# Optimization experiments

Measured on AMD Instinct MI355X. Metric: run time of the kernel, lower is better.

The kernel has to match this reference:

```python
import jax, jax.numpy as jnp
import numpy as np

DIM = 512
HEADS = 8
HD = DIM // HEADS
B, T, N = 4, 64, 196
HIDDEN = 2048  # dim * ffn_ratio
SCALE = HD ** -0.5
EPS = 1e-5


def _ln(x, g, b):
    m = jnp.mean(x, axis=-1, keepdims=True)
    v = jnp.mean(jnp.square(x - m), axis=-1, keepdims=True)
    return (x - m) / jnp.sqrt(v + EPS) * g + b


def _attn(x, qkv_w, q_b, v_b, proj_w, proj_b, mask=None):
    # x: [B', T', N', C]; attention over the N' axis
    Bp, Tp, Np, C = x.shape
    bias = jnp.concatenate([q_b, jnp.zeros_like(v_b), v_b])  # torch cat(q_bias, zeros, v_bias)
    qkv = x @ qkv_w.T + bias                                  # [B',T',N',3C]
    qkv = qkv.reshape(Bp, Tp, Np, 3, HEADS, HD).transpose(3, 0, 1, 4, 2, 5)
    q, k, v = qkv[0] * SCALE, qkv[1], qkv[2]                  # [B',T',H,N',hd]
    attn = jnp.einsum('bthnd,bthmd->bthnm', q, k)             # [B',T',H,N',N']
    if mask is not None:
        attn = attn + mask                                    # broadcast [N',N'] bias
    attn = jax.nn.softmax(attn, axis=-1)
    out = jnp.einsum('bthnm,bthmd->bthnd', attn, v)
    out = out.transpose(0, 1, 3, 2, 4).reshape(Bp, Tp, Np, C)
    return out @ proj_w.T + proj_b


def setup_inputs() -> dict:
    key = jax.random.key(0)
    ks = jax.random.split(key, 16)
    w = lambda k, s: (0.02 * jax.random.normal(k, s)).astype(jnp.float32)
    return {
        'x': jax.random.normal(ks[0], (B, T, N, DIM), dtype=jnp.float32),
        'mask': 0.1 * jax.random.normal(ks[1], (T, T), dtype=jnp.float32),
        'n1_g': jnp.ones((DIM,), jnp.float32),
        'n1_b': jnp.zeros((DIM,), jnp.float32),
        's_qkv_w': w(ks[2], (3 * DIM, DIM)),
        's_q_b': jnp.zeros((DIM,), jnp.float32),
        's_v_b': jnp.zeros((DIM,), jnp.float32),
        's_proj_w': w(ks[3], (DIM, DIM)),
        's_proj_b': jnp.zeros((DIM,), jnp.float32),
        't_qkv_w': w(ks[4], (3 * DIM, DIM)),
        't_q_b': jnp.zeros((DIM,), jnp.float32),
        't_v_b': jnp.zeros((DIM,), jnp.float32),
        't_proj_w': w(ks[5], (DIM, DIM)),
        't_proj_b': jnp.zeros((DIM,), jnp.float32),
        'n2_g': jnp.ones((DIM,), jnp.float32),
        'n2_b': jnp.zeros((DIM,), jnp.float32),
        'ffn_w1': w(ks[6], (HIDDEN, DIM)),
        'ffn_b1': jnp.zeros((HIDDEN,), jnp.float32),
        'ffn_w2': w(ks[7], (DIM, HIDDEN)),
        'ffn_b2': jnp.zeros((DIM,), jnp.float32),
    }


def reference(x, mask, n1_g, n1_b, s_qkv_w, s_q_b, s_v_b, s_proj_w, s_proj_b,
              t_qkv_w, t_q_b, t_v_b, t_proj_w, t_proj_b,
              n2_g, n2_b, ffn_w1, ffn_b1, ffn_w2, ffn_b2):
    h = _ln(x, n1_g, n1_b)
    sp = _attn(h, s_qkv_w, s_q_b, s_v_b, s_proj_w, s_proj_b)
    # temporal branch: transpose (B,T,N,C) -> (B,N,T,C); mask [T,T] biases the T x T scores
    tm = _attn(h.transpose(0, 2, 1, 3), t_qkv_w, t_q_b, t_v_b, t_proj_w, t_proj_b, mask)
    tm = tm.transpose(0, 2, 1, 3)
    x = x + 0.5 * sp + 0.5 * tm
    h2 = _ln(x, n2_g, n2_b)
    ffn = jax.nn.gelu(h2 @ ffn_w1.T + ffn_b1, approximate=False) @ ffn_w2.T + ffn_b2
    return x + ffn
```

## Files before the change

kernel.cpp:

```cpp
#include <hip/hip_runtime.h>
#include <cmath>

typedef unsigned short u16;
typedef __bf16 bf16x8 __attribute__((ext_vector_type(8)));
typedef float f32x4 __attribute__((ext_vector_type(4)));

__device__ __forceinline__ float bflo(unsigned u){ return __uint_as_float(u << 16); }
__device__ __forceinline__ float bfhi(unsigned u){ return __uint_as_float(u & 0xffff0000u); }
__device__ __forceinline__ float b2f(u16 b){ return __uint_as_float(((unsigned)b) << 16); }
__device__ __forceinline__ u16 f2bf(float f){
  unsigned u = __float_as_uint(f);
  u = u + 0x7fffu + ((u >> 16) & 1u);
  return (u16)(u >> 16);
}
__device__ __forceinline__ unsigned pk2(float a, float b){
  return (unsigned)f2bf(a) | ((unsigned)f2bf(b) << 16);
}
__device__ __forceinline__ void up8(uint4 u, float* f){
  f[0]=bflo(u.x); f[1]=bfhi(u.x); f[2]=bflo(u.y); f[3]=bfhi(u.y);
  f[4]=bflo(u.z); f[5]=bfhi(u.z); f[6]=bflo(u.w); f[7]=bfhi(u.w);
}
__device__ __forceinline__ float rdd(const void* p, int f, size_t i){
  return f ? ((const float*)p)[i] : b2f(((const u16*)p)[i]);
}
__device__ __forceinline__ float erf_fast(float x){
  const float ax = fabsf(x);
  const float t  = __builtin_amdgcn_rcpf(1.f + 0.3275911f * ax);
  float p = 1.061405429f;
  p = p * t - 1.453152027f;
  p = p * t + 1.421413741f;
  p = p * t - 0.284496736f;
  p = p * t + 0.254829592f;
  const float e = __expf(-ax * ax);
  const float r = 1.f - p * t * e;
  return copysignf(r, x);
}
__device__ __forceinline__ void gload16(const u16* g, u16* l){
  __builtin_amdgcn_global_load_lds(
      (const __attribute__((address_space(1))) void*)g,
      (__attribute__((address_space(3))) void*)l, 16, 0, 0);
}

__global__ void detect_k(const unsigned* __restrict__ n1g, int* __restrict__ flag){
  if (threadIdx.x == 0 && blockIdx.x == 0)
    *flag = (n1g[0] == 0x3F800000u) ? 1 : 0;
}

__global__ void conv_k(const void* __restrict__ src, u16* __restrict__ dst, int n,
                       const int* __restrict__ flag){
  const int f = *flag;
  const int i = blockIdx.x * 256 + threadIdx.x;
  if (i >= n) return;
  dst[i] = f ? f2bf(((const float*)src)[i]) : ((const u16*)src)[i];
}

__global__ void conv_multi(const void* a0, const void* a1, const void* a2, const void* a3,
                           const void* a4, const void* a5, const void* a6, const void* a7,
                           const void* a8, const void* a9, const void* aa, const void* ab,
                           const void* ac, u16* __restrict__ dst, const int* __restrict__ flag){
  const int f = *flag;
  const int i = blockIdx.x * 256 + threadIdx.x;
  if (i >= 11776) return;
  const void* s; int o;
  if      (i < 2048)  { s = a0; o = i; }
  else if (i < 2560)  { s = a1; o = i - 2048; }
  else if (i < 3072)  { s = a2; o = i - 2560; }
  else if (i < 3584)  { s = a3; o = i - 3072; }
  else if (i < 4096)  { s = a4; o = i - 3584; }
  else if (i < 4608)  { s = a5; o = i - 4096; }
  else if (i < 8704)  { s = a6; o = i - 4608; }
  else if (i < 9216)  { s = a7; o = i - 8704; }
  else if (i < 9728)  { s = a8; o = i - 9216; }
  else if (i < 10240) { s = a9; o = i - 9728; }
  else if (i < 10752) { s = aa; o = i - 10240; }
  else if (i < 11264) { s = ab; o = i - 10752; }
  else                { s = ac; o = i - 11264; }
  dst[i] = f ? f2bf(((const float*)s)[o]) : ((const u16*)s)[o];
}

__global__ void build_bias(const u16* __restrict__ sqb, const u16* __restrict__ svb,
                           const u16* __restrict__ tqb, const u16* __restrict__ tvb,
                           u16* __restrict__ dst){
  int i = blockIdx.x * 256 + threadIdx.x;
  if (i >= 1536) return;
  u16 s, t;
  if (i < 512)       { s = sqb[i];       t = tqb[i]; }
  else if (i < 1024) { s = 0;            t = 0; }
  else               { s = svb[i-1024];  t = tvb[i-1024]; }
  dst[i] = s; dst[1536 + i] = t;
}

__global__ void build_cproj(const void* __restrict__ sp, const void* __restrict__ tp,
                            const void* __restrict__ spb, const void* __restrict__ tpb,
                            u16* __restrict__ wc, u16* __restrict__ cb,
                            const int* __restrict__ flag){
  const int f = *flag;
  const int i = blockIdx.x * 256 + threadIdx.x;
  if (i < 524288){
    const int n = i >> 10, k = i & 1023;
    const float v = (k < 512) ? rdd(sp, f, (size_t)n*512 + k)
                              : rdd(tp, f, (size_t)n*512 + k - 512);
    wc[i] = f2bf(v);
  }
  if (i < 512) cb[i] = f2bf(rdd(spb, f, i) + rdd(tpb, f, i));
}

__global__ __launch_bounds__(256) void ln_k(const void* __restrict__ x, int rowbase,
                                            const u16* __restrict__ g, const u16* __restrict__ b,
                                            u16* __restrict__ out, const int* __restrict__ flagp){
  const int f = *flagp;
  const int gw   = (blockIdx.x * 256 + threadIdx.x) >> 6;
  const int lane = threadIdx.x & 63;
  const size_t base = (size_t)(rowbase + gw) * 512 + lane * 8;
  float fv[8];
  if (f){
    const float4* p = (const float4*)((const float*)x + base);
    float4 a = p[0], c = p[1];
    fv[0]=a.x; fv[1]=a.y; fv[2]=a.z; fv[3]=a.w;
    fv[4]=c.x; fv[5]=c.y; fv[6]=c.z; fv[7]=c.w;
  } else {
    up8(*(const uint4*)((const u16*)x + base), fv);
  }
  float s1 = 0.f, s2 = 0.f;
  #pragma unroll
  for (int i = 0; i < 8; i++){ s1 += fv[i]; s2 += fv[i]*fv[i]; }
  #pragma unroll
  for (int off = 32; off > 0; off >>= 1){
    s1 += __shfl_xor(s1, off, 64);
    s2 += __shfl_xor(s2, off, 64);
  }
  const float mean = s1 * (1.f/512.f);
  const float var  = fmaxf(s2 * (1.f/512.f) - mean*mean, 0.f);
  const float inv  = rsqrtf(var + 1e-5f);
  float gg[8], bb[8];
  up8(*(const uint4*)&g[lane*8], gg);
  up8(*(const uint4*)&b[lane*8], bb);
  float r[8];
  #pragma unroll
  for (int i = 0; i < 8; i++) r[i] = (fv[i]-mean)*inv*gg[i] + bb[i];
  uint4 o;
  o.x = pk2(r[0],r[1]); o.y = pk2(r[2],r[3]); o.z = pk2(r[4],r[5]); o.w = pk2(r[6],r[7]);
  *(uint4*)&out[(size_t)gw*512 + lane*8] = o;
}

template<int EPI, int IO>
__global__ __launch_bounds__(512, 6) void gemm_bt(
    const u16* __restrict__ A, const u16* __restrict__ W, int ldw,
    const u16* __restrict__ bias, const void* __restrict__ res,
    void* __restrict__ out, int rowbase, int N, int K, const int* __restrict__ flagp)
{
  __shared__ u16 sA[2][128 * 32];
  __shared__ u16 sB[2][128 * 32];
  const int f = (IO == 1) ? *flagp : 0;
  const int tid  = threadIdx.x;
  const int wave = tid >> 6, lane = tid & 63;
  const int wm   = (wave >> 1) * 32;
  const int wn   = (wave & 1) * 64;
  const int col0 = blockIdx.x * 128, row0 = blockIdx.y * 128;

  f32x4 acc[2][4];
  const f32x4 z = {0.f, 0.f, 0.f, 0.f};
  #pragma unroll
  for (int i = 0; i < 2; i++)
    #pragma unroll
    for (int j = 0; j < 4; j++) acc[i][j] = z;

  const int srow = (wave << 4) + (lane >> 2);
  const int scol = (lane & 3) * 8;
  const u16* Ag = A + (size_t)(row0 + srow) * K   + scol;
  const u16* Wg = W + (size_t)(col0 + srow) * ldw + scol;
  const int wofs = wave << 9;
  const int ks = (lane >> 4) * 8, mr = lane & 15;

  #define STAGE(bb, kk) do {                    \
    gload16(Ag + (kk), &sA[bb][wofs]);          \
    gload16(Wg + (kk), &sB[bb][wofs]);          \
  } while (0)

  const int nit = K >> 5;
  STAGE(0, 0);
  for (int it = 0; it < nit; ++it){
    const int b = it & 1;
    if (it + 1 < nit){
      STAGE(b ^ 1, (it + 1) << 5);
      asm volatile("s_waitcnt vmcnt(2)" ::: "memory");
    } else {
      asm volatile("s_waitcnt vmcnt(0)" ::: "memory");
    }
    __builtin_amdgcn_s_barrier();
    bf16x8 af[2], bq[4];
    #pragma unroll
    for (int i = 0; i < 2; i++)
      af[i] = *(const bf16x8*)&sA[b][(wm + i*16 + mr)*32 + ks];
    #pragma unroll
    for (int j = 0; j < 4; j++)
      bq[j] = *(const bf16x8*)&sB[b][(wn + j*16 + mr)*32 + ks];
    #pragma unroll
    for (int i = 0; i < 2; i++)
      #pragma unroll
      for (int j = 0; j < 4; j++)
        acc[i][j] = __builtin_amdgcn_mfma_f32_16x16x32_bf16(bq[j], af[i], acc[i][j], 0, 0, 0);
    __builtin_amdgcn_s_barrier();
  }
  #undef STAGE

  #pragma unroll
  for (int i = 0; i < 2; i++){
    const int m = row0 + wm + i*16 + mr;
    const size_t rowoff = (size_t)(rowbase + m) * N;
    #pragma unroll
    for (int j = 0; j < 4; j++){
      const int n0 = col0 + wn + j*16 + (lane >> 4)*4;
      const uint2 bb = *(const uint2*)&bias[n0];
      float v[4];
      v[0] = acc[i][j][0] + bflo(bb.x);
      v[1] = acc[i][j][1] + bfhi(bb.x);
      v[2] = acc[i][j][2] + bflo(bb.y);
      v[3] = acc[i][j][3] + bfhi(bb.y);
      if (EPI == 1 || EPI == 3){
        float r4[4];
        if (f){
          const float4 rr = *(const float4*)((const float*)res + rowoff + n0);
          r4[0]=rr.x; r4[1]=rr.y; r4[2]=rr.z; r4[3]=rr.w;
        } else {
          const uint2 ru = *(const uint2*)((const u16*)res + rowoff + n0);
          r4[0]=bflo(ru.x); r4[1]=bfhi(ru.x); r4[2]=bflo(ru.y); r4[3]=bfhi(ru.y);
        }
        #pragma unroll
        for (int t = 0; t < 4; t++)
          v[t] = (EPI == 1) ? r4[t] + 0.5f * v[t] : r4[t] + v[t];
      } else if (EPI == 2){
        #pragma unroll
        for (int t = 0; t < 4; t++)
          v[t] = 0.5f * v[t] * (1.f + erf_fast(v[t] * 0.70710678f));
      }
      if (IO == 0 || !f){
        uint2 o; o.x = pk2(v[0], v[1]); o.y = pk2(v[2], v[3]);
        *(uint2*)((u16*)out + rowoff + n0) = o;
      } else {
        float4 o = {v[0], v[1], v[2], v[3]};
        *(float4*)((float*)out + rowoff + n0) = o;
      }
    }
  }
}

#define VSTR 232
__global__ __launch_bounds__(256) void attn_spatial_mfma(const u16* __restrict__ qkv, int rstr,
                                                         u16* __restrict__ ao, int ostr){
  __shared__ u16 Vt[64 * VSTR];
  __shared__ u16 Ps[4][16 * VSTR];
  const int btl = blockIdx.x, h = blockIdx.y;
  const u16* base = qkv + (size_t)btl * 196 * rstr + h * 64;
  const int tid = threadIdx.x, wave = tid >> 6, lane = tid & 63;
  const f32x4 z4 = {0.f, 0.f, 0.f, 0.f};

  for (int tsk = tid; tsk < 1568; tsk += 256){
    const int m = tsk >> 3, d8 = (tsk & 7) * 8;
    float vf[8];
    up8(*(const uint4*)&base[(size_t)m*rstr + 1024 + d8], vf);
    #pragma unroll
    for (int j = 0; j < 8; j++) Vt[(d8 + j)*VSTR + m] = f2bf(vf[j]);
  }
  for (int tsk = tid; tsk < 64*28; tsk += 256){
    const int d = tsk / 28, m = 196 + (tsk - d*28);
    Vt[d*VSTR + m] = 0;
  }
  __syncthreads();

  const int li = lane & 15, q8 = (lane >> 4) * 8;
  for (int p = 0; p < 4; p++){
    const int rt = p*4 + wave;
    if (rt > 12) continue;
    const int row0 = rt * 16;
    const int qrc = min(row0 + li, 195);
    const u16* qp = base + (size_t)qrc*rstr + q8;
    const bf16x8 q0 = *(const bf16x8*)qp;
    const bf16x8 q1 = *(const bf16x8*)(qp + 32);

    f32x4 acc[14];
    #pragma unroll
    for (int mt = 0; mt < 14; mt++) acc[mt] = z4;
    #pragma unroll
    for (int mt = 0; mt < 14; mt++){
      const int krc = min(mt*16 + li, 195);
      const u16* kp = base + (size_t)krc*rstr + 512 + q8;
      const bf16x8 k0 = *(const bf16x8*)kp;
      const bf16x8 k1 = *(const bf16x8*)(kp + 32);
      acc[mt] = __builtin_amdgcn_mfma_f32_16x16x32_bf16(q0, k0, acc[mt], 0, 0, 0);
      acc[mt] = __builtin_amdgcn_mfma_f32_16x16x32_bf16(q1, k1, acc[mt], 0, 0, 0);
    }
    float den[4];
    #pragma unroll
    for (int rr = 0; rr < 4; rr++){
      float mx = -1.0e30f;
      #pragma unroll
      for (int mt = 0; mt < 14; mt++){
        float s = acc[mt][rr] * 0.125f;
        if (mt*16 + li >= 196) s = -1.0e30f;
        acc[mt][rr] = s;
        mx = fmaxf(mx, s);
      }
      #pragma unroll
      for (int off = 1; off < 16; off <<= 1) mx = fmaxf(mx, __shfl_xor(mx, off, 64));
      float d = 0.f;
      #pragma unroll
      for (int mt = 0; mt < 14; mt++){
        const float pv = __expf(acc[mt][rr] - mx);
        acc[mt][rr] = pv;
        d += pv;
      }
      #pragma unroll
      for (int off = 1; off < 16; off <<= 1) d += __shfl_xor(d, off, 64);
      den[rr] = d;
    }
    u16* ps = &Ps[wave][0];
    #pragma unroll
    for (int rr = 0; rr < 4; rr++){
      const int prow = (lane >> 4)*4 + rr;
      #pragma unroll
      for (int mt = 0; mt < 14; mt++)
        ps[prow*VSTR + mt*16 + li] = f2bf(acc[mt][rr]);
    }
    f32x4 ov[4];
    #pragma unroll
    for (int nt = 0; nt < 4; nt++) ov[nt] = z4;
    #pragma unroll
    for (int kk = 0; kk < 7; kk++){
      const bf16x8 pf = *(const bf16x8*)&ps[li*VSTR + kk*32 + q8];
      #pragma unroll
      for (int nt = 0; nt < 4; nt++){
        const bf16x8 vb = *(const bf16x8*)&Vt[(nt*16 + li)*VSTR + kk*32 + q8];
        ov[nt] = __builtin_amdgcn_mfma_f32_16x16x32_bf16(pf, vb, ov[nt], 0, 0, 0);
      }
    }
    #pragma unroll
    for (int rr = 0; rr < 4; rr++){
      const int row = row0 + (lane >> 4)*4 + rr;
      if (row < 196){
        const float inv = 1.f / den[rr];
        u16* orow = ao + ((size_t)btl*196 + row)*ostr + h*64;
        #pragma unroll
        for (int nt = 0; nt < 4; nt++)
          orow[nt*16 + li] = f2bf(ov[nt][rr] * inv);
      }
    }
  }
}

#define TSTR 72
__global__ __launch_bounds__(256) void attn_temporal_mfma(const u16* __restrict__ qkv, int rstr,
                                                          const u16* __restrict__ mask,
                                                          u16* __restrict__ ao, int ostr){
  __shared__ u16 Ks[64 * TSTR];
  __shared__ u16 Vt[64 * TSTR];
  __shared__ u16 Mk[64 * TSTR];
  __shared__ u16 Ps[4][16 * TSTR];
  const int n = blockIdx.x, h = blockIdx.y, bz = blockIdx.z;
  const int tid = threadIdx.x, wave = tid >> 6, lane = tid & 63;
  const size_t trow = (size_t)196 * rstr;
  const u16* base = qkv + ((size_t)bz*12544 + n) * rstr + h * 64;
  const f32x4 z4 = {0.f, 0.f, 0.f, 0.f};

  for (int tsk = tid; tsk < 512; tsk += 256){
    const int r = tsk >> 3, c8 = (tsk & 7) * 8;
    *(uint4*)&Ks[r*TSTR + c8] = *(const uint4*)&base[(size_t)r*trow + 512 + c8];
    *(uint4*)&Mk[r*TSTR + c8] = *(const uint4*)&mask[r*64 + c8];
    float vf[8];
    up8(*(const uint4*)&base[(size_t)r*trow + 1024 + c8], vf);
    #pragma unroll
    for (int j = 0; j < 8; j++) Vt[(c8 + j)*TSTR + r] = f2bf(vf[j]);
  }
  __syncthreads();

  const int li = lane & 15, q8 = (lane >> 4) * 8;
  const int row0 = wave * 16;
  const u16* qp = base + (size_t)(row0 + li)*trow + q8;
  const bf16x8 q0 = *(const bf16x8*)qp;
  const bf16x8 q1 = *(const bf16x8*)(qp + 32);

  f32x4 acc[4];
  #pragma unroll
  for (int mt = 0; mt < 4; mt++) acc[mt] = z4;
  #pragma unroll
  for (int mt = 0; mt < 4; mt++){
    const bf16x8 k0 = *(const bf16x8*)&Ks[(mt*16 + li)*TSTR + q8];
    const bf16x8 k1 = *(const bf16x8*)&Ks[(mt*16 + li)*TSTR + 32 + q8];
    acc[mt] = __builtin_amdgcn_mfma_f32_16x16x32_bf16(q0, k0, acc[mt], 0, 0, 0);
    acc[mt] = __builtin_amdgcn_mfma_f32_16x16x32_bf16(q1, k1, acc[mt], 0, 0, 0);
  }
  float den[4];
  #pragma unroll
  for (int rr = 0; rr < 4; rr++){
    const int tq = row0 + (lane >> 4)*4 + rr;
    float mx = -1.0e30f;
    #pragma unroll
    for (int mt = 0; mt < 4; mt++){
      const float s = acc[mt][rr] * 0.125f + b2f(Mk[tq*TSTR + mt*16 + li]);
      acc[mt][rr] = s;
      mx = fmaxf(mx, s);
    }
    #pragma unroll
    for (int off = 1; off < 16; off <<= 1) mx = fmaxf(mx, __shfl_xor(mx, off, 64));
    float d = 0.f;
    #pragma unroll
    for (int mt = 0; mt < 4; mt++){
      const float pv = __expf(acc[mt][rr] - mx);
      acc[mt][rr] = pv;
      d += pv;
    }
    #pragma unroll
    for (int off = 1; off < 16; off <<= 1) d += __shfl_xor(d, off, 64);
    den[rr] = d;
  }
  u16* ps = &Ps[wave][0];
  #pragma unroll
  for (int rr = 0; rr < 4; rr++){
    const int prow = (lane >> 4)*4 + rr;
    #pragma unroll
    for (int mt = 0; mt < 4; mt++)
      ps[prow*TSTR + mt*16 + li] = f2bf(acc[mt][rr]);
  }
  f32x4 ov[4];
  #pragma unroll
  for (int nt = 0; nt < 4; nt++) ov[nt] = z4;
  #pragma unroll
  for (int kk = 0; kk < 2; kk++){
    const bf16x8 pf = *(const bf16x8*)&ps[li*TSTR + kk*32 + q8];
    #pragma unroll
    for (int nt = 0; nt < 4; nt++){
      const bf16x8 vb = *(const bf16x8*)&Vt[(nt*16 + li)*TSTR + kk*32 + q8];
      ov[nt] = __builtin_amdgcn_mfma_f32_16x16x32_bf16(pf, vb, ov[nt], 0, 0, 0);
    }
  }
  #pragma unroll
  for (int rr = 0; rr < 4; rr++){
    const int tq = row0 + (lane >> 4)*4 + rr;
    const float inv = 1.f / den[rr];
    u16* orow = ao + ((size_t)bz*12544 + (size_t)tq*196 + n)*ostr + h*64;
    #pragma unroll
    for (int nt = 0; nt < 4; nt++)
      orow[nt*16 + li] = f2bf(ov[nt][rr] * inv);
  }
}

extern "C" void kernel_launch(void* const* d_in, const int* in_sizes, int n_in,
                              void* d_out, int out_size, void* d_ws, size_t ws_size,
                              hipStream_t stream)
{
  (void)in_sizes; (void)n_in; (void)out_size;
  const void* x = d_in[0];
  void* outp = d_out;

  u16* ws = (u16*)d_ws;
  u16* m_sqkvw = ws;
  u16* m_tqkvw = ws + 786432;
  u16* m_sprojw= ws + 1572864;
  u16* m_tprojw= ws + 1835008;
  u16* m_cprojw= ws + 2097152;
  u16* m_fw1   = ws + 2621440;
  u16* m_fw2   = ws + 3670016;
  u16* m_fb1   = ws + 4718592;
  u16* m_fb2   = ws + 4720640;
  u16* m_n1g   = ws + 4721152;
  u16* m_n1b   = ws + 4721664;
  u16* m_n2g   = ws + 4722176;
  u16* m_n2b   = ws + 4722688;
  u16* m_mask  = ws + 4723200;
  u16* m_sqb   = ws + 4727296;
  u16* m_svb   = ws + 4727808;
  u16* m_tqb   = ws + 4728320;
  u16* m_tvb   = ws + 4728832;
  u16* m_spb   = ws + 4729344;
  u16* m_tpb   = ws + 4729856;
  u16* m_cpb   = ws + 4730368;
  u16* bias2   = ws + 4730880;
  int* flag    = (int*)(ws + 4733952);
  u16* buf     = ws + 4734016;

  const size_t MIR = 4734016;
  #define NEED(CHX) ((MIR + (size_t)(CHX)*4608) * 2)
  int CHX;
  if      (ws_size >= NEED(50176)) CHX = 50176;
  else if (ws_size >= NEED(25088)) CHX = 25088;
  else if (ws_size >= NEED(12544)) CHX = 12544;
  else                             CHX = 0;
  #undef NEED

  detect_k<<<dim3(1), dim3(64), 0, stream>>>((const unsigned*)d_in[2], flag);
  conv_multi<<<dim3(46), dim3(256), 0, stream>>>(
      d_in[17], d_in[19], d_in[2], d_in[3], d_in[14], d_in[15], d_in[1],
      d_in[5], d_in[6], d_in[10], d_in[11], d_in[8], d_in[13], m_fb1, flag);
  #define CONV(idx, dst, n) conv_k<<<dim3(((n)+255)/256), dim3(256), 0, stream>>>(d_in[idx], dst, n, flag)
  CONV(4,  m_sqkvw, 786432);
  CONV(9,  m_tqkvw, 786432);
  CONV(7,  m_sprojw,262144);
  CONV(12, m_tprojw,262144);
  CONV(16, m_fw1,  1048576);
  CONV(18, m_fw2,  1048576);
  #undef CONV
  build_bias<<<dim3(6), dim3(256), 0, stream>>>(m_sqb, m_svb, m_tqb, m_tvb, bias2);
  build_cproj<<<dim3(2048), dim3(256), 0, stream>>>(d_in[7], d_in[12], d_in[8], d_in[13],
                                                    m_cprojw, m_cpb, flag);

  if (CHX > 0){
    const int nb = CHX / 12544;
    const int nc = 50176 / CHX;
    const int gr = CHX / 128;
    const int sp = CHX / 196;
    u16* hc  = buf;
    u16* qq  = buf + (size_t)CHX*512;
    u16* ao  = buf + (size_t)CHX*3584;
    u16* mid = qq;
    for (int c = 0; c < nc; c++){
      const int rb = c * CHX;
      ln_k<<<dim3(CHX/4), dim3(256), 0, stream>>>(x, rb, m_n1g, m_n1b, hc, flag);
      gemm_bt<0,0><<<dim3(24, gr), dim3(512), 0, stream>>>(hc, m_sqkvw, 512, bias2, nullptr, qq, 0, 3072, 512, flag);
      attn_spatial_mfma<<<dim3(sp, 8), dim3(256), 0, stream>>>(qq, 3072, ao, 1024);
      attn_temporal_mfma<<<dim3(196, 8, nb), dim3(256), 0, stream>>>(qq + 1536, 3072, m_mask, ao + 512, 1024);
      gemm_bt<1,1><<<dim3(4, gr), dim3(512), 0, stream>>>(ao, m_cprojw, 1024, m_cpb, x, outp, rb, 512, 1024, flag);
      ln_k<<<dim3(CHX/4), dim3(256), 0, stream>>>(outp, rb, m_n2g, m_n2b, hc, flag);
      gemm_bt<2,0><<<dim3(16, gr), dim3(512), 0, stream>>>(hc, m_fw1, 512, m_fb1, nullptr, mid, 0, 2048, 512, flag);
      gemm_bt<3,1><<<dim3(4, gr), dim3(512), 0, stream>>>(mid, m_fw2, 2048, m_fb2, outp, outp, rb, 512, 2048, flag);
    }
  } else {
    const int CH = 12544;
    u16* hc  = buf;
    u16* Wq  = buf + (size_t)CH*512;
    u16* Wa  = buf + (size_t)CH*2048;
    u16* mid = Wq;
    for (int c = 0; c < 4; c++){
      const int rb = c * CH;
      ln_k<<<dim3(3136), dim3(256), 0, stream>>>(x, rb, m_n1g, m_n1b, hc, flag);
      gemm_bt<0,0><<<dim3(12, 98), dim3(512), 0, stream>>>(hc, m_sqkvw, 512, bias2, nullptr, Wq, 0, 1536, 512, flag);
      attn_spatial_mfma<<<dim3(64, 8), dim3(256), 0, stream>>>(Wq, 1536, Wa, 512);
      gemm_bt<1,1><<<dim3(4, 98), dim3(512), 0, stream>>>(Wa, m_sprojw, 512, m_spb, x, outp, rb, 512, 512, flag);
      gemm_bt<0,0><<<dim3(12, 98), dim3(512), 0, stream>>>(hc, m_tqkvw, 512, bias2 + 1536, nullptr, Wq, 0, 1536, 512, flag);
      attn_temporal_mfma<<<dim3(196, 8, 1), dim3(256), 0, stream>>>(Wq, 1536, m_mask, Wa, 512);
      gemm_bt<1,1><<<dim3(4, 98), dim3(512), 0, stream>>>(Wa, m_tprojw, 512, m_tpb, outp, outp, rb, 512, 512, flag);
      ln_k<<<dim3(3136), dim3(256), 0, stream>>>(outp, rb, m_n2g, m_n2b, hc, flag);
      gemm_bt<2,0><<<dim3(16, 98), dim3(512), 0, stream>>>(hc, m_fw1, 512, m_fb1, nullptr, mid, 0, 2048, 512, flag);
      gemm_bt<3,1><<<dim3(4, 98), dim3(512), 0, stream>>>(mid, m_fw2, 2048, m_fb2, outp, outp, rb, 512, 2048, flag);
    }
  }
}
```

Before: 1.276 ms.

## Enlarge GEMM tile to 256x128 and swizzle LDS columns

The bf16 MFMA GEMM now computes a 256x128 tile per block, so each wave owns a 64x64 sub-tile with 16 accumulators instead of 8, and the grid row count is halved accordingly. This raises arithmetic intensity per LDS fragment load and per global load of the weight tile. An XOR swizzle on the k-column offset within LDS rows is added to reduce bank conflicts on fragment reads. The cost is more registers per thread (launch bounds lowered to 4) and fewer blocks, which can hurt occupancy and tail balance on small grids.

```diff
diff --git a/kernel.cpp b/kernel.cpp
--- a/kernel.cpp
+++ b/kernel.cpp
@@ -144,37 +144,41 @@
 }
 
 template<int EPI, int IO>
-__global__ __launch_bounds__(512, 6) void gemm_bt(
+__global__ __launch_bounds__(512, 4) void gemm_bt(
     const u16* __restrict__ A, const u16* __restrict__ W, int ldw,
     const u16* __restrict__ bias, const void* __restrict__ res,
     void* __restrict__ out, int rowbase, int N, int K, const int* __restrict__ flagp)
 {
-  __shared__ u16 sA[2][128 * 32];
+  __shared__ u16 sA[2][256 * 32];
   __shared__ u16 sB[2][128 * 32];
   const int f = (IO == 1) ? *flagp : 0;
   const int tid  = threadIdx.x;
   const int wave = tid >> 6, lane = tid & 63;
-  const int wm   = (wave >> 1) * 32;
-  const int wn   = (wave & 1) * 64;
-  const int col0 = blockIdx.x * 128, row0 = blockIdx.y * 128;
-
-  f32x4 acc[2][4];
+  const int wr   = (wave >> 1) * 64;
+  const int wc   = (wave & 1) * 64;
+  const int col0 = blockIdx.x * 128, row0 = blockIdx.y * 256;
+
+  f32x4 acc[4][4];
   const f32x4 z = {0.f, 0.f, 0.f, 0.f};
   #pragma unroll
-  for (int i = 0; i < 2; i++)
+  for (int i = 0; i < 4; i++)
     #pragma unroll
     for (int j = 0; j < 4; j++) acc[i][j] = z;
 
-  const int srow = (wave << 4) + (lane >> 2);
-  const int scol = (lane & 3) * 8;
-  const u16* Ag = A + (size_t)(row0 + srow) * K   + scol;
-  const u16* Wg = W + (size_t)(col0 + srow) * ldw + scol;
-  const int wofs = wave << 9;
-  const int ks = (lane >> 4) * 8, mr = lane & 15;
-
-  #define STAGE(bb, kk) do {                    \
-    gload16(Ag + (kk), &sA[bb][wofs]);          \
-    gload16(Wg + (kk), &sB[bb][wofs]);          \
+  const int srow = lane >> 2;
+  const int scol = ((lane & 3) ^ ((lane >> 3) & 3)) * 8;
+  const u16* Ag = A + (size_t)(row0 + (wave << 5) + srow) * K + scol;
+  const u16* Wg = W + (size_t)(col0 + (wave << 4) + srow) * ldw + scol;
+  const size_t ajmp = (size_t)16 * K;
+  const int wofsA = wave << 10;
+  const int wofsB = wave << 9;
+  const int ksw = (((lane >> 4) ^ ((lane >> 1) & 3)) * 8);
+  const int mr = lane & 15;
+
+  #define STAGE(bb, kk) do {                              \
+    gload16(Ag + (kk),        &sA[bb][wofsA]);            \
+    gload16(Ag + (kk) + ajmp, &sA[bb][wofsA + 512]);      \
+    gload16(Wg + (kk),        &sB[bb][wofsB]);            \
   } while (0)
 
   const int nit = K >> 5;
@@ -183,20 +187,20 @@
     const int b = it & 1;
     if (it + 1 < nit){
       STAGE(b ^ 1, (it + 1) << 5);
-      asm volatile("s_waitcnt vmcnt(2)" ::: "memory");
+      asm volatile("s_waitcnt vmcnt(3)" ::: "memory");
     } else {
       asm volatile("s_waitcnt vmcnt(0)" ::: "memory");
     }
     __builtin_amdgcn_s_barrier();
-    bf16x8 af[2], bq[4];
-    #pragma unroll
-    for (int i = 0; i < 2; i++)
-      af[i] = *(const bf16x8*)&sA[b][(wm + i*16 + mr)*32 + ks];
+    bf16x8 af[4], bq[4];
+    #pragma unroll
+    for (int i = 0; i < 4; i++)
+      af[i] = *(const bf16x8*)&sA[b][(wr + i*16 + mr)*32 + ksw];
     #pragma unroll
     for (int j = 0; j < 4; j++)
-      bq[j] = *(const bf16x8*)&sB[b][(wn + j*16 + mr)*32 + ks];
-    #pragma unroll
-    for (int i = 0; i < 2; i++)
+      bq[j] = *(const bf16x8*)&sB[b][(wc + j*16 + mr)*32 + ksw];
+    #pragma unroll
+    for (int i = 0; i < 4; i++)
       #pragma unroll
       for (int j = 0; j < 4; j++)
         acc[i][j] = __builtin_amdgcn_mfma_f32_16x16x32_bf16(bq[j], af[i], acc[i][j], 0, 0, 0);
@@ -205,12 +209,12 @@
   #undef STAGE
 
   #pragma unroll
-  for (int i = 0; i < 2; i++){
-    const int m = row0 + wm + i*16 + mr;
+  for (int i = 0; i < 4; i++){
+    const int m = row0 + wr + i*16 + mr;
     const size_t rowoff = (size_t)(rowbase + m) * N;
     #pragma unroll
     for (int j = 0; j < 4; j++){
-      const int n0 = col0 + wn + j*16 + (lane >> 4)*4;
+      const int n0 = col0 + wc + j*16 + (lane >> 4)*4;
       const uint2 bb = *(const uint2*)&bias[n0];
       float v[4];
       v[0] = acc[i][j][0] + bflo(bb.x);
@@ -506,7 +510,7 @@
   if (CHX > 0){
     const int nb = CHX / 12544;
     const int nc = 50176 / CHX;
-    const int gr = CHX / 128;
+    const int gr = CHX / 256;
     const int sp = CHX / 196;
     u16* hc  = buf;
     u16* qq  = buf + (size_t)CHX*512;
@@ -532,15 +536,15 @@
     for (int c = 0; c < 4; c++){
       const int rb = c * CH;
       ln_k<<<dim3(3136), dim3(256), 0, stream>>>(x, rb, m_n1g, m_n1b, hc, flag);
-      gemm_bt<0,0><<<dim3(12, 98), dim3(512), 0, stream>>>(hc, m_sqkvw, 512, bias2, nullptr, Wq, 0, 1536, 512, flag);
+      gemm_bt<0,0><<<dim3(12, 49), dim3(512), 0, stream>>>(hc, m_sqkvw, 512, bias2, nullptr, Wq, 0, 1536, 512, flag);
       attn_spatial_mfma<<<dim3(64, 8), dim3(256), 0, stream>>>(Wq, 1536, Wa, 512);
-      gemm_bt<1,1><<<dim3(4, 98), dim3(512), 0, stream>>>(Wa, m_sprojw, 512, m_spb, x, outp, rb, 512, 512, flag);
-      gemm_bt<0,0><<<dim3(12, 98), dim3(512), 0, stream>>>(hc, m_tqkvw, 512, bias2 + 1536, nullptr, Wq, 0, 1536, 512, flag);
+      gemm_bt<1,1><<<dim3(4, 49), dim3(512), 0, stream>>>(Wa, m_sprojw, 512, m_spb, x, outp, rb, 512, 512, flag);
+      gemm_bt<0,0><<<dim3(12, 49), dim3(512), 0, stream>>>(hc, m_tqkvw, 512, bias2 + 1536, nullptr, Wq, 0, 1536, 512, flag);
       attn_temporal_mfma<<<dim3(196, 8, 1), dim3(256), 0, stream>>>(Wq, 1536, m_mask, Wa, 512);
-      gemm_bt<1,1><<<dim3(4, 98), dim3(512), 0, stream>>>(Wa, m_tprojw, 512, m_tpb, outp, outp, rb, 512, 512, flag);
+      gemm_bt<1,1><<<dim3(4, 49), dim3(512), 0, stream>>>(Wa, m_tprojw, 512, m_tpb, outp, outp, rb, 512, 512, flag);
       ln_k<<<dim3(3136), dim3(256), 0, stream>>>(outp, rb, m_n2g, m_n2b, hc, flag);
-      gemm_bt<2,0><<<dim3(16, 98), dim3(512), 0, stream>>>(hc, m_fw1, 512, m_fb1, nullptr, mid, 0, 2048, 512, flag);
-      gemm_bt<3,1><<<dim3(4, 98), dim3(512), 0, stream>>>(mid, m_fw2, 2048, m_fb2, outp, outp, rb, 512, 2048, flag);
-    }
-  }
-}
+      gemm_bt<2,0><<<dim3(16, 49), dim3(512), 0, stream>>>(hc, m_fw1, 512, m_fb1, nullptr, mid, 0, 2048, 512, flag);
+      gemm_bt<3,1><<<dim3(4, 49), dim3(512), 0, stream>>>(mid, m_fw2, 2048, m_fb2, outp, outp, rb, 512, 2048, flag);
+    }
+  }
+}
```

Measured after the change: 1.137 ms. 10.9% less time.
